# Performance work log

Hardware: AMD Instinct MI355X
Metric: run time of the kernel (lower is better)

## Reference

```python
import jax, jax.numpy as jnp
import numpy as np
from jax import lax

B, T, D, H, L, F, K, G = 4, 1024, 1024, 16, 4, 4096, 128, 16
HD = D // H
EPS = 1e-5

def _ln(x, s, b):
    m = jnp.mean(x, axis=-1, keepdims=True)
    v = jnp.mean(jnp.square(x - m), axis=-1, keepdims=True)
    return (x - m) * lax.rsqrt(v + EPS) * s + b

def setup_inputs() -> dict:
    key = jax.random.key(0)
    ks = jax.random.split(key, 16)
    s = 0.02
    rn = lambda k, sh: jax.random.normal(k, sh, dtype=jnp.float32)
    return {
        "x": rn(ks[0], (B, T, D)),
        "position_bias": rn(ks[1], (H, T, T)) * 0.1,
        "conv_w": rn(ks[2], (D, D // G, K)) * s,  # torch Conv1d OIH layout
        "conv_b": jnp.zeros((D,), jnp.float32),
        "ln0_s": jnp.ones((D,), jnp.float32),
        "ln0_b": jnp.zeros((D,), jnp.float32),
        "qkv_w": rn(ks[3], (L, D, 3 * D)) * s,
        "qkv_b": jnp.zeros((L, 3 * D), jnp.float32),
        "out_w": rn(ks[4], (L, D, D)) * s,
        "out_b": jnp.zeros((L, D), jnp.float32),
        "gru_w": rn(ks[5], (L, HD, 8)) * s,
        "gru_b": jnp.zeros((L, 8), jnp.float32),
        "gru_c": jnp.ones((L, 1, H, 1, 1), jnp.float32),
        "ln1_s": jnp.ones((L, D), jnp.float32),
        "ln1_b": jnp.zeros((L, D), jnp.float32),
        "ffn_w1": rn(ks[6], (L, D, F)) * s,
        "ffn_b1": jnp.zeros((L, F), jnp.float32),
        "ffn_w2": rn(ks[7], (L, F, D)) * s,
        "ffn_b2": jnp.zeros((L, D), jnp.float32),
        "ln2_s": jnp.ones((L, D), jnp.float32),
        "ln2_b": jnp.zeros((L, D), jnp.float32),
    }

def _conv_pos(x, conv_w, conv_b):
    # x: (B, T, D) -> ConvPositionalEmbedding (non-causal): pad K//2, drop last (K even), GELU
    xc = x.transpose(0, 2, 1)  # (B, D, T)
    y = lax.conv_general_dilated(
        xc, conv_w, window_strides=(1,), padding=[(K // 2, K // 2)],
        dimension_numbers=("NCH", "OIH", "NCH"), feature_group_count=G)
    y = y[..., :-1] + conv_b[None, :, None]  # remove=1 since kernel even
    return jax.nn.gelu(y, approximate=False).transpose(0, 2, 1)

def _layer(x, position_bias, qkv_w, qkv_b, out_w, out_b, gru_w, gru_b, gru_c,
           ln1_s, ln1_b, ffn_w1, ffn_b1, ffn_w2, ffn_b2, ln2_s, ln2_b):
    b, t, _ = x.shape
    qkv = x @ qkv_w + qkv_b                       # (B, T, 3D)
    qkv = qkv.reshape(b, t, 3, H, HD)
    q, k, v = (qkv[:, :, i].transpose(0, 2, 1, 3) for i in range(3))  # (B,H,T,HD)
    # GRU-gated relative position bias
    gi = x.reshape(b, t, H, HD).transpose(0, 2, 1, 3)      # (B,H,T,HD)
    proj = (gi @ gru_w + gru_b).reshape(b, H, t, 2, 4).sum(-1)  # (B,H,T,2)
    g = jax.nn.sigmoid(proj)
    gate_a, gate_b = g[..., :1], g[..., 1:]
    gate = gate_a * (gate_b * gru_c - 1.0) + 2.0            # (B,H,T,1)
    gated_bias = gate * position_bias                       # (B,H,T,T)
    scores = jnp.einsum("bhqd,bhkd->bhqk", q, k) / np.sqrt(HD) + gated_bias
    attn = jax.nn.softmax(scores, axis=-1)
    o = jnp.einsum("bhqk,bhkd->bhqd", attn, v)
    o = o.transpose(0, 2, 1, 3).reshape(b, t, D) @ out_w + out_b
    x = _ln(x + o, ln1_s, ln1_b)
    f = jax.nn.gelu(x @ ffn_w1 + ffn_b1, approximate=False) @ ffn_w2 + ffn_b2
    return _ln(x + f, ln2_s, ln2_b)

def reference(x, position_bias, conv_w, conv_b, ln0_s, ln0_b, qkv_w, qkv_b,
              out_w, out_b, gru_w, gru_b, gru_c, ln1_s, ln1_b,
              ffn_w1, ffn_b1, ffn_w2, ffn_b2, ln2_s, ln2_b):
    x = x + _conv_pos(x, conv_w, conv_b)
    x = _ln(x, ln0_s, ln0_b)
    for i in range(L):
        x = _layer(x, position_bias, qkv_w[i], qkv_b[i], out_w[i], out_b[i],
                   gru_w[i], gru_b[i], gru_c[i], ln1_s[i], ln1_b[i],
                   ffn_w1[i], ffn_b1[i], ffn_w2[i], ffn_b2[i], ln2_s[i], ln2_b[i])
    return x
```

## Files before the change

kernel.cpp:

```cpp
#include <hip/hip_runtime.h>
#include <hip/hip_bf16.h>
#include <math.h>

#define B_ 4
#define T_ 1024
#define D_ 1024
#define H_ 16
#define HD_ 64
#define L_ 4
#define F_ 4096
#define KC_ 128
#define G_ 16

typedef __attribute__((ext_vector_type(8))) short bf16x8;
typedef __attribute__((ext_vector_type(4))) float f32x4;

__device__ __forceinline__ float bf2f(unsigned short h){ return __uint_as_float(((unsigned int)h)<<16); }
__device__ __forceinline__ unsigned short f2bf(float f){
  unsigned int u = __float_as_uint(f);
  unsigned int r = u + 0x7fffu + ((u>>16)&1u);
  return (unsigned short)(r>>16);
}
__device__ __forceinline__ float gelu_exact(float v){ return 0.5f*v*(1.0f+erff(v*0.70710678118654752f)); }
__device__ __forceinline__ bool is_f32d(const unsigned short* disc){ return disc[0] == 0; }
__device__ __forceinline__ float dynload(const void* p, long long i, bool f32){
  return f32 ? ((const float*)p)[i] : bf2f(((const unsigned short*)p)[i]);
}
__device__ __forceinline__ void gl2lds16(const void* g, void* l){
  __builtin_amdgcn_global_load_lds((const __attribute__((address_space(1))) void*)g,
                                   (__attribute__((address_space(3))) void*)l, 16, 0, 0);
}

__global__ __launch_bounds__(256)
void cvt_bf16(const void* __restrict__ src, unsigned short* __restrict__ dst,
              const unsigned short* __restrict__ disc)
{
  const bool f32 = is_f32d(disc);
  long long i0 = ((long long)blockIdx.x*256 + threadIdx.x)*8;
  if (f32){
    #pragma unroll
    for (int j=0;j<8;j++) dst[i0+j] = f2bf(((const float*)src)[i0+j]);
  } else {
    *(uint4*)&dst[i0] = *(const uint4*)(&((const unsigned short*)src)[i0]);
  }
}

template<int ACT>
__global__ __launch_bounds__(256)
void gemm_bt(const unsigned short* __restrict__ A, long long lda,
             const unsigned short* __restrict__ Bt, long long ldb,
             unsigned short* __restrict__ C, long long ldc,
             const void* __restrict__ bias,
             const unsigned short* __restrict__ disc, long long biasOff,
             int M, int N, int Kd,
             long long aZ, long long bZ, long long cZ)
{
  A  += (long long)blockIdx.z * aZ;
  Bt += (long long)blockIdx.z * bZ;
  C  += (long long)blockIdx.z * cZ;
  const int n0 = blockIdx.x * 128;
  const int m0 = blockIdx.y * 128;
  __shared__ unsigned short As[128*32];
  __shared__ unsigned short Bs[128*32];
  const int tid  = threadIdx.x;
  const int lane = tid & 63;
  const int wave = tid >> 6;
  const int wm = (wave >> 1) * 64;
  const int wn = (wave & 1) * 64;
  const int lm = lane & 15;
  const int lq = lane >> 4;
  f32x4 acc[4][4];
  #pragma unroll
  for (int i=0;i<4;i++)
    #pragma unroll
    for (int j=0;j<4;j++) acc[i][j] = (f32x4){0.f,0.f,0.f,0.f};

  const int sr = tid >> 2;
  const int sk = (tid & 3) * 8;
  for (int k0 = 0; k0 < Kd; k0 += 32) {
    __syncthreads();
    int b0r = n0 + sr;      if (b0r > N-1) b0r = N-1;
    int b1r = n0 + 64 + sr; if (b1r > N-1) b1r = N-1;
    gl2lds16(&A [(long long)(m0 + sr)      * lda + k0 + sk], &As[tid*8]);
    gl2lds16(&A [(long long)(m0 + 64 + sr) * lda + k0 + sk], &As[2048 + tid*8]);
    gl2lds16(&Bt[(long long)b0r * ldb + k0 + sk],            &Bs[tid*8]);
    gl2lds16(&Bt[(long long)b1r * ldb + k0 + sk],            &Bs[2048 + tid*8]);
    __syncthreads();
    bf16x8 af[4], bfr[4];
    #pragma unroll
    for (int i=0;i<4;i++){
      af[i]  = *(const bf16x8*)&As[(wm + i*16 + lm)*32 + lq*8];
      bfr[i] = *(const bf16x8*)&Bs[(wn + i*16 + lm)*32 + lq*8];
    }
    #pragma unroll
    for (int mi=0;mi<4;mi++)
      #pragma unroll
      for (int ni=0;ni<4;ni++)
        acc[mi][ni] = __builtin_amdgcn_mfma_f32_16x16x32_bf16(af[mi], bfr[ni], acc[mi][ni], 0, 0, 0);
  }
  const bool f32 = is_f32d(disc);
  #pragma unroll
  for (int ni=0;ni<4;ni++){
    int gn = n0 + wn + ni*16 + lm;
    if (gn >= N) continue;
    float bv = bias ? dynload(bias, biasOff + gn, f32) : 0.f;
    #pragma unroll
    for (int mi=0;mi<4;mi++){
      int gm = m0 + wm + mi*16 + lq*4;
      #pragma unroll
      for (int r=0;r<4;r++){
        float v = acc[mi][ni][r] + bv;
        if (ACT==1) v = gelu_exact(v);
        C[(long long)(gm + r) * ldc + gn] = f2bf(v);
      }
    }
  }
}

__global__ __launch_bounds__(256)
void transpose2d(const void* __restrict__ in, long long irs, long long inZ,
                 unsigned short* __restrict__ out, long long ors, long long outZ,
                 const unsigned short* __restrict__ disc, long long eoff)
{
  const bool f32 = disc ? is_f32d(disc) : false;
  const unsigned short* in16 = (const unsigned short*)in;
  const float* in32 = (const float*)in;
  const long long zoff = eoff + (long long)blockIdx.z * inZ;
  out += (long long)blockIdx.z * outZ;
  __shared__ unsigned short tile[64][65];
  const int c0 = blockIdx.x * 64;
  const int r0 = blockIdx.y * 64;
  const int tid = threadIdx.x;
  const int tr = tid >> 4;
  const int tc = (tid & 15) * 4;
  #pragma unroll
  for (int i=0;i<4;i++){
    long long base = zoff + (long long)(r0 + tr + i*16) * irs + c0 + tc;
    #pragma unroll
    for (int j=0;j<4;j++)
      tile[tr + i*16][tc+j] = f32 ? f2bf(in32[base+j]) : in16[base+j];
  }
  __syncthreads();
  #pragma unroll
  for (int i=0;i<4;i++){
    unsigned short* q = out + (long long)(c0 + tr + i*16) * ors + r0 + tc;
    q[0] = tile[tc+0][tr + i*16];
    q[1] = tile[tc+1][tr + i*16];
    q[2] = tile[tc+2][tr + i*16];
    q[3] = tile[tc+3][tr + i*16];
  }
}

__global__ __launch_bounds__(256)
void convw_transform(const void* __restrict__ cw, unsigned short* __restrict__ cwT,
                     const unsigned short* __restrict__ disc)
{
  const bool f32 = is_f32d(disc);
  const int o = blockIdx.x;
  __shared__ unsigned short lds[8192];
  const long long base = (long long)o*8192;
  for (int idx=threadIdx.x; idx<8192; idx+=256)
    lds[idx] = f32 ? f2bf(((const float*)cw)[base+idx]) : ((const unsigned short*)cw)[base+idx];
  __syncthreads();
  for (int idx=threadIdx.x; idx<8192; idx+=256){
    int k = idx >> 6, ic = idx & 63;
    cwT[((long long)k<<16) + (o<<6) + ic] = lds[ic*128 + k];
  }
}

__global__ __launch_bounds__(256)
void conv_mfma(const unsigned short* __restrict__ x,
               const unsigned short* __restrict__ cwT,
               const void* __restrict__ cb,
               unsigned short* __restrict__ out,
               const unsigned short* __restrict__ disc)
{
  const int g  = blockIdx.x;
  const int t0 = blockIdx.y * 128;
  const int b  = blockIdx.z;
  __shared__ unsigned short xs[255*72];
  __shared__ unsigned short wbuf[2*64*72];
  const int tid  = threadIdx.x;
  const int lane = tid & 63;
  const int wave = tid >> 6;
  const int lm = lane & 15;
  const int lq = lane >> 4;

  for (int c = tid; c < 255*8; c += 256){
    int row = c >> 3, icc = (c & 7) * 8;
    int t = t0 - 64 + row;
    uint4 v = {0,0,0,0};
    if (t >= 0 && t < T_) v = *(const uint4*)&x[((long long)b*T_ + t)*D_ + (g<<6) + icc];
    *(uint4*)&xs[row*72 + icc] = v;
  }

  f32x4 acc[2][4];
  #pragma unroll
  for (int i=0;i<2;i++)
    #pragma unroll
    for (int j=0;j<4;j++) acc[i][j] = (f32x4){0.f,0.f,0.f,0.f};

  uint4 wreg[4];
  #pragma unroll
  for (int j=0;j<4;j++){
    int cc = j*256 + tid;
    int tapL = cc >> 9, rem = cc & 511;
    wreg[j] = *(const uint4*)&cwT[((long long)tapL<<16) + (g<<12) + rem*8];
  }

  for (int it = 0; it < 64; it++){
    __syncthreads();
    #pragma unroll
    for (int j=0;j<4;j++){
      int cc = j*256 + tid;
      int tapL = cc >> 9, rem = cc & 511;
      int o = rem >> 3, icc = (rem & 7) * 8;
      *(uint4*)&wbuf[(tapL*64 + o)*72 + icc] = wreg[j];
    }
    __syncthreads();
    if (it < 63){
      int tapBase = (it+1)*2;
      #pragma unroll
      for (int j=0;j<4;j++){
        int cc = j*256 + tid;
        int tapL = cc >> 9, rem = cc & 511;
        wreg[j] = *(const uint4*)&cwT[((long long)(tapBase+tapL)<<16) + (g<<12) + rem*8];
      }
    }
    #pragma unroll
    for (int tl=0; tl<2; tl++){
      int tap = it*2 + tl;
      #pragma unroll
      for (int ks=0; ks<2; ks++){
        bf16x8 a0 = *(const bf16x8*)&xs[(wave*32      + lm + tap)*72 + ks*32 + lq*8];
        bf16x8 a1 = *(const bf16x8*)&xs[(wave*32 + 16 + lm + tap)*72 + ks*32 + lq*8];
        #pragma unroll
        for (int ni=0; ni<4; ni++){
          bf16x8 bf = *(const bf16x8*)&wbuf[(tl*64 + ni*16 + lm)*72 + ks*32 + lq*8];
          acc[0][ni] = __builtin_amdgcn_mfma_f32_16x16x32_bf16(a0, bf, acc[0][ni], 0, 0, 0);
          acc[1][ni] = __builtin_amdgcn_mfma_f32_16x16x32_bf16(a1, bf, acc[1][ni], 0, 0, 0);
        }
      }
    }
  }

  const bool f32 = is_f32d(disc);
  float bv[4];
  #pragma unroll
  for (int ni=0; ni<4; ni++) bv[ni] = dynload(cb, (g<<6) + ni*16 + lm, f32);
  #pragma unroll
  for (int mt=0; mt<2; mt++){
    #pragma unroll
    for (int r=0; r<4; r++){
      int t = t0 + wave*32 + mt*16 + lq*4 + r;
      long long base = ((long long)b*T_ + t)*D_ + (g<<6);
      #pragma unroll
      for (int ni=0; ni<4; ni++){
        int o = ni*16 + lm;
        float val = acc[mt][ni][r] + bv[ni];
        float xv  = bf2f(x[base + o]);
        out[base + o] = f2bf(xv + gelu_exact(val));
      }
    }
  }
}

__global__ __launch_bounds__(256)
void add_ln(const unsigned short* __restrict__ a,
            const unsigned short* __restrict__ bAdd,
            const void* __restrict__ s, const void* __restrict__ bi,
            void* __restrict__ out,
            const unsigned short* __restrict__ disc, int dynOut, long long eoff)
{
  const bool f32 = is_f32d(disc);
  const long long row = blockIdx.x;
  const int tid = threadIdx.x;
  __shared__ float red[8];
  float v[4];
  uint2 ua = *(const uint2*)&a[row*D_ + tid*4];
  unsigned short t4[4]; *(uint2*)t4 = ua;
  v[0]=bf2f(t4[0]); v[1]=bf2f(t4[1]); v[2]=bf2f(t4[2]); v[3]=bf2f(t4[3]);
  if (bAdd){
    uint2 ub = *(const uint2*)&bAdd[row*D_ + tid*4];
    *(uint2*)t4 = ub;
    v[0]+=bf2f(t4[0]); v[1]+=bf2f(t4[1]); v[2]+=bf2f(t4[2]); v[3]+=bf2f(t4[3]);
  }
  float sum = v[0]+v[1]+v[2]+v[3];
  float sq  = v[0]*v[0]+v[1]*v[1]+v[2]*v[2]+v[3]*v[3];
  #pragma unroll
  for (int off=32; off>=1; off>>=1){
    sum += __shfl_xor(sum, off);
    sq  += __shfl_xor(sq,  off);
  }
  const int wv = tid>>6;
  if ((tid&63)==0){ red[wv] = sum; red[4+wv] = sq; }
  __syncthreads();
  sum = red[0]+red[1]+red[2]+red[3];
  sq  = red[4]+red[5]+red[6]+red[7];
  float mean = sum * (1.0f/D_);
  float var  = sq * (1.0f/D_) - mean*mean;
  float rstd = rsqrtf(var + 1e-5f);
  #pragma unroll
  for (int i=0;i<4;i++){
    float sv = dynload(s, eoff + tid*4+i, f32);
    float bv = dynload(bi, eoff + tid*4+i, f32);
    float ov = (v[i]-mean)*rstd*sv + bv;
    if (dynOut && f32) ((float*)out)[row*D_ + tid*4 + i] = ov;
    else ((unsigned short*)out)[row*D_ + tid*4 + i] = f2bf(ov);
  }
}

__global__ __launch_bounds__(256)
void gate_kernel(const unsigned short* __restrict__ x,
                 const void* __restrict__ gw, const void* __restrict__ gb,
                 const void* __restrict__ gc, float* __restrict__ gate,
                 const unsigned short* __restrict__ disc,
                 long long wOff, long long bOff, long long cOff)
{
  const bool f32 = is_f32d(disc);
  int r = blockIdx.x*4 + (threadIdx.x>>6);
  int lane = threadIdx.x & 63;
  int b = r >> 14;
  int h = (r >> 10) & 15;
  int t = r & 1023;
  float xv = bf2f(x[((long long)b*T_ + t)*D_ + h*64 + lane]);
  float w0=0.f, w1=0.f;
  #pragma unroll
  for (int j=0;j<4;j++) w0 += dynload(gw, wOff + lane*8+j, f32);
  #pragma unroll
  for (int j=4;j<8;j++) w1 += dynload(gw, wOff + lane*8+j, f32);
  float p0 = xv*w0, p1 = xv*w1;
  #pragma unroll
  for (int off=32; off>=1; off>>=1){
    p0 += __shfl_xor(p0, off);
    p1 += __shfl_xor(p1, off);
  }
  if (lane==0){
    float b0=0.f, b1=0.f;
    #pragma unroll
    for (int j=0;j<4;j++) b0 += dynload(gb, bOff + j, f32);
    #pragma unroll
    for (int j=4;j<8;j++) b1 += dynload(gb, bOff + j, f32);
    float s0 = p0 + b0, s1 = p1 + b1;
    float ga  = 1.f/(1.f+expf(-s0));
    float gbv = 1.f/(1.f+expf(-s1));
    float c = dynload(gc, cOff + h, f32);
    gate[r] = ga*(gbv*c - 1.0f) + 2.0f;
  }
}

__global__ __launch_bounds__(256)
void attn_fused(const unsigned short* __restrict__ qkv,
                const unsigned short* __restrict__ vT,
                const void* __restrict__ pb,
                const float* __restrict__ gate,
                unsigned short* __restrict__ o,
                const unsigned short* __restrict__ disc)
{
  const int q0 = blockIdx.x * 64;
  const int h  = blockIdx.y;
  const int b  = blockIdx.z;
  const bool f32 = is_f32d(disc);
  __shared__ unsigned short Ks[64*72];
  __shared__ unsigned short Vs[64*72];
  __shared__ unsigned short Ps[64*72];
  const int tid  = threadIdx.x;
  const int lane = tid & 63;
  const int wave = tid >> 6;
  const int lm = lane & 15;
  const int lq = lane >> 4;

  bf16x8 qa[2];
  {
    const unsigned short* qrow = &qkv[((long long)b*T_ + q0 + wave*16 + lm)*3*D_ + h*64];
    qa[0] = *(const bf16x8*)&qrow[lq*8];
    qa[1] = *(const bf16x8*)&qrow[32 + lq*8];
  }
  float g4[4];
  #pragma unroll
  for (int r=0;r<4;r++)
    g4[r] = gate[((long long)(b*H_ + h))*T_ + q0 + wave*16 + lq*4 + r];

  float m[4] = {-3.0e38f,-3.0e38f,-3.0e38f,-3.0e38f};
  float l[4] = {0.f,0.f,0.f,0.f};
  f32x4 oacc[4];
  #pragma unroll
  for (int ni=0;ni<4;ni++) oacc[ni] = (f32x4){0.f,0.f,0.f,0.f};

  const unsigned short* kbase = &qkv[((long long)b*T_)*3*D_ + D_ + h*64];
  const unsigned short* vtb   = &vT[((long long)b*H_ + h)*64*T_];
  const long long pbrow = ((long long)h*T_ + q0 + wave*16 + lq*4)*T_;

  for (int kv0 = 0; kv0 < T_; kv0 += 64){
    __syncthreads();
    #pragma unroll
    for (int jj=0; jj<2; jj++){
      int cc = jj*256 + tid;
      int row = cc >> 3, icc = (cc & 7)*8;
      *(uint4*)&Ks[row*72 + icc] = *(const uint4*)&kbase[(long long)(kv0+row)*3*D_ + icc];
    }
    #pragma unroll
    for (int jj=0; jj<2; jj++){
      int cc = jj*256 + tid;
      int row = cc >> 3, icc = (cc & 7)*8;
      *(uint4*)&Vs[row*72 + icc] = *(const uint4*)&vtb[(long long)row*T_ + kv0 + icc];
    }
    __syncthreads();
    f32x4 s[4];
    #pragma unroll
    for (int ni=0;ni<4;ni++){
      s[ni] = (f32x4){0.f,0.f,0.f,0.f};
      bf16x8 kb0 = *(const bf16x8*)&Ks[(ni*16+lm)*72 + lq*8];
      bf16x8 kb1 = *(const bf16x8*)&Ks[(ni*16+lm)*72 + 32 + lq*8];
      s[ni] = __builtin_amdgcn_mfma_f32_16x16x32_bf16(qa[0], kb0, s[ni], 0, 0, 0);
      s[ni] = __builtin_amdgcn_mfma_f32_16x16x32_bf16(qa[1], kb1, s[ni], 0, 0, 0);
    }
    #pragma unroll
    for (int ni=0;ni<4;ni++)
      #pragma unroll
      for (int r=0;r<4;r++)
        s[ni][r] = s[ni][r]*0.125f + g4[r]*dynload(pb, pbrow + (long long)r*T_ + kv0 + ni*16 + lm, f32);
    #pragma unroll
    for (int r=0;r<4;r++){
      float mx = fmaxf(fmaxf(s[0][r],s[1][r]), fmaxf(s[2][r],s[3][r]));
      mx = fmaxf(mx, __shfl_xor(mx,1));
      mx = fmaxf(mx, __shfl_xor(mx,2));
      mx = fmaxf(mx, __shfl_xor(mx,4));
      mx = fmaxf(mx, __shfl_xor(mx,8));
      float mn = fmaxf(m[r], mx);
      float sc = __expf(m[r]-mn);
      m[r] = mn;
      float rs = 0.f;
      #pragma unroll
      for (int ni=0;ni<4;ni++){
        float e = __expf(s[ni][r]-mn);
        s[ni][r] = e;
        rs += e;
      }
      rs += __shfl_xor(rs,1); rs += __shfl_xor(rs,2);
      rs += __shfl_xor(rs,4); rs += __shfl_xor(rs,8);
      l[r] = l[r]*sc + rs;
      #pragma unroll
      for (int ni=0;ni<4;ni++) oacc[ni][r] *= sc;
    }
    #pragma unroll
    for (int ni=0;ni<4;ni++)
      #pragma unroll
      for (int r=0;r<4;r++)
        Ps[(wave*16+lq*4+r)*72 + ni*16+lm] = f2bf(s[ni][r]);
    bf16x8 pa0 = *(const bf16x8*)&Ps[(wave*16+lm)*72 + lq*8];
    bf16x8 pa1 = *(const bf16x8*)&Ps[(wave*16+lm)*72 + 32 + lq*8];
    #pragma unroll
    for (int ni=0;ni<4;ni++){
      bf16x8 vb0 = *(const bf16x8*)&Vs[(ni*16+lm)*72 + lq*8];
      bf16x8 vb1 = *(const bf16x8*)&Vs[(ni*16+lm)*72 + 32 + lq*8];
      oacc[ni] = __builtin_amdgcn_mfma_f32_16x16x32_bf16(pa0, vb0, oacc[ni], 0, 0, 0);
      oacc[ni] = __builtin_amdgcn_mfma_f32_16x16x32_bf16(pa1, vb1, oacc[ni], 0, 0, 0);
    }
  }
  #pragma unroll
  for (int r=0;r<4;r++){
    float inv = 1.0f / l[r];
    int q = q0 + wave*16 + lq*4 + r;
    #pragma unroll
    for (int ni=0;ni<4;ni++)
      o[((long long)b*T_ + q)*D_ + h*64 + ni*16 + lm] = f2bf(oacc[ni][r]*inv);
  }
}

extern "C" void kernel_launch(void* const* d_in, const int* in_sizes, int n_in,
                              void* d_out, int out_size, void* d_ws, size_t ws_size,
                              hipStream_t stream)
{
  (void)in_sizes; (void)n_in; (void)out_size; (void)ws_size;
  const void* x_in     = d_in[0];
  const void* pos_bias = d_in[1];
  const void* conv_w   = d_in[2];
  const void* conv_b   = d_in[3];
  const unsigned short* disc = (const unsigned short*)d_in[4];
  const void* ln0_s    = d_in[4];
  const void* ln0_b    = d_in[5];
  const void* qkv_w    = d_in[6];
  const void* qkv_b    = d_in[7];
  const void* out_w    = d_in[8];
  const void* out_b    = d_in[9];
  const void* gru_w    = d_in[10];
  const void* gru_b    = d_in[11];
  const void* gru_c    = d_in[12];
  const void* ln1_s    = d_in[13];
  const void* ln1_b    = d_in[14];
  const void* ffn_w1   = d_in[15];
  const void* ffn_b1   = d_in[16];
  const void* ffn_w2   = d_in[17];
  const void* ffn_b2   = d_in[18];
  const void* ln2_s    = d_in[19];
  const void* ln2_b    = d_in[20];

  const size_t MB = (size_t)1<<20;
  char* ws = (char*)d_ws;
  unsigned short* xcvt   = (unsigned short*)(ws);
  unsigned short* xbuf   = (unsigned short*)(ws +   8*MB);
  unsigned short* qkvbuf = (unsigned short*)(ws +  16*MB);
  unsigned short* obuf   = (unsigned short*)(ws +  40*MB);
  unsigned short* hs     = (unsigned short*)(ws +  48*MB);
  unsigned short* wT     = (unsigned short*)(ws +  80*MB);
  float*          gateb  = (float*)         (ws + 106*MB);

  dim3 blk(256);

  cvt_bf16<<<dim3((B_*T_*D_)/2048), blk, 0, stream>>>(x_in, xcvt, disc);
  convw_transform<<<dim3(1024), blk, 0, stream>>>(conv_w, wT, disc);
  conv_mfma<<<dim3(G_, T_/128, B_), blk, 0, stream>>>(xcvt, wT, conv_b, xbuf, disc);
  add_ln<<<dim3(B_*T_), blk, 0, stream>>>(xbuf, nullptr, ln0_s, ln0_b, xbuf, disc, 0, 0);

  for (int l=0; l<L_; l++){
    unsigned short* qkvT = wT;
    unsigned short* outT = wT + (size_t)3*1024*1024;
    unsigned short* w1T  = wT + (size_t)4*1024*1024;
    unsigned short* w2T  = wT + (size_t)8*1024*1024;
    unsigned short* vTall = hs;
    transpose2d<<<dim3(48,16,1), blk, 0, stream>>>(qkv_w, 3*D_, 0, qkvT, D_, 0, disc, (long long)l*D_*3*D_);
    transpose2d<<<dim3(16,16,1), blk, 0, stream>>>(out_w, D_,   0, outT, D_, 0, disc, (long long)l*D_*D_);
    transpose2d<<<dim3(64,16,1), blk, 0, stream>>>(ffn_w1, F_,  0, w1T,  D_, 0, disc, (long long)l*D_*F_);
    transpose2d<<<dim3(16,64,1), blk, 0, stream>>>(ffn_w2, D_,  0, w2T,  F_, 0, disc, (long long)l*F_*D_);

    gate_kernel<<<dim3(B_*H_*T_/4), blk, 0, stream>>>(xbuf, gru_w, gru_b, gru_c, gateb, disc,
                                                      (long long)l*HD_*8, (long long)l*8, (long long)l*H_);

    gemm_bt<0><<<dim3(24,32,1), blk, 0, stream>>>(xbuf, D_, qkvT, D_, qkvbuf, 3*D_, qkv_b, disc, (long long)l*3*D_,
                                                  B_*T_, 3*D_, D_, 0,0,0);
    for (int b=0;b<B_;b++)
      transpose2d<<<dim3(1,16,16), blk, 0, stream>>>(qkvbuf + (long long)b*T_*3*D_ + 2*D_, 3*D_, 64,
                                                     vTall + (long long)b*H_*64*T_, T_, (long long)64*T_,
                                                     nullptr, 0);
    attn_fused<<<dim3(T_/64, H_, B_), blk, 0, stream>>>(qkvbuf, vTall, pos_bias, gateb, obuf, disc);

    gemm_bt<0><<<dim3(8,32,1), blk, 0, stream>>>(obuf, D_, outT, D_, qkvbuf, D_, out_b, disc, (long long)l*D_,
                                                 B_*T_, D_, D_, 0,0,0);
    add_ln<<<dim3(B_*T_), blk, 0, stream>>>(xbuf, qkvbuf, ln1_s, ln1_b, xbuf, disc, 0, (long long)l*D_);
    gemm_bt<1><<<dim3(32,32,1), blk, 0, stream>>>(xbuf, D_, w1T, D_, hs, F_, ffn_b1, disc, (long long)l*F_,
                                                  B_*T_, F_, D_, 0,0,0);
    gemm_bt<0><<<dim3(8,32,1), blk, 0, stream>>>(hs, F_, w2T, F_, qkvbuf, D_, ffn_b2, disc, (long long)l*D_,
                                                 B_*T_, D_, F_, 0,0,0);
    void* dst = (l==L_-1) ? d_out : (void*)xbuf;
    add_ln<<<dim3(B_*T_), blk, 0, stream>>>(xbuf, qkvbuf, ln2_s, ln2_b, dst, disc, (l==L_-1)?1:0, (long long)l*D_);
  }
}
```

Measured before the change: 2.254 ms.

## Fuse gate, conversion and transposes into fewer launches; add 128x64 GEMM tile

New measurement: 1.875 ms. 16.8% less time.

```diff
diff --git a/kernel.cpp b/kernel.cpp
--- a/kernel.cpp
+++ b/kernel.cpp
@@ -29,20 +29,6 @@
 __device__ __forceinline__ void gl2lds16(const void* g, void* l){
   __builtin_amdgcn_global_load_lds((const __attribute__((address_space(1))) void*)g,
                                    (__attribute__((address_space(3))) void*)l, 16, 0, 0);
-}
-
-__global__ __launch_bounds__(256)
-void cvt_bf16(const void* __restrict__ src, unsigned short* __restrict__ dst,
-              const unsigned short* __restrict__ disc)
-{
-  const bool f32 = is_f32d(disc);
-  long long i0 = ((long long)blockIdx.x*256 + threadIdx.x)*8;
-  if (f32){
-    #pragma unroll
-    for (int j=0;j<8;j++) dst[i0+j] = f2bf(((const float*)src)[i0+j]);
-  } else {
-    *(uint4*)&dst[i0] = *(const uint4*)(&((const unsigned short*)src)[i0]);
-  }
 }
 
 template<int ACT>
@@ -117,25 +103,96 @@
   }
 }
 
-__global__ __launch_bounds__(256)
-void transpose2d(const void* __restrict__ in, long long irs, long long inZ,
-                 unsigned short* __restrict__ out, long long ors, long long outZ,
-                 const unsigned short* __restrict__ disc, long long eoff)
-{
-  const bool f32 = disc ? is_f32d(disc) : false;
+template<int ACT>
+__global__ __launch_bounds__(256)
+void gemm_bt64(const unsigned short* __restrict__ A, long long lda,
+               const unsigned short* __restrict__ Bt, long long ldb,
+               unsigned short* __restrict__ C, long long ldc,
+               const void* __restrict__ bias,
+               const unsigned short* __restrict__ disc, long long biasOff,
+               int M, int N, int Kd)
+{
+  const int n0 = blockIdx.x * 64;
+  const int m0 = blockIdx.y * 128;
+  __shared__ unsigned short As[128*32];
+  __shared__ unsigned short Bs[64*32];
+  const int tid  = threadIdx.x;
+  const int lane = tid & 63;
+  const int wave = tid >> 6;
+  const int wm = wave * 32;
+  const int lm = lane & 15;
+  const int lq = lane >> 4;
+  f32x4 acc[2][4];
+  #pragma unroll
+  for (int i=0;i<2;i++)
+    #pragma unroll
+    for (int j=0;j<4;j++) acc[i][j] = (f32x4){0.f,0.f,0.f,0.f};
+
+  const int sr = tid >> 2;
+  const int sk = (tid & 3) * 8;
+  for (int k0 = 0; k0 < Kd; k0 += 32) {
+    __syncthreads();
+    gl2lds16(&A [(long long)(m0 + sr)      * lda + k0 + sk], &As[tid*8]);
+    gl2lds16(&A [(long long)(m0 + 64 + sr) * lda + k0 + sk], &As[2048 + tid*8]);
+    gl2lds16(&Bt[(long long)(n0 + sr)      * ldb + k0 + sk], &Bs[tid*8]);
+    __syncthreads();
+    bf16x8 af[2], bfr[4];
+    #pragma unroll
+    for (int i=0;i<2;i++) af[i]  = *(const bf16x8*)&As[(wm + i*16 + lm)*32 + lq*8];
+    #pragma unroll
+    for (int i=0;i<4;i++) bfr[i] = *(const bf16x8*)&Bs[(i*16 + lm)*32 + lq*8];
+    #pragma unroll
+    for (int mi=0;mi<2;mi++)
+      #pragma unroll
+      for (int ni=0;ni<4;ni++)
+        acc[mi][ni] = __builtin_amdgcn_mfma_f32_16x16x32_bf16(af[mi], bfr[ni], acc[mi][ni], 0, 0, 0);
+  }
+  const bool f32 = is_f32d(disc);
+  #pragma unroll
+  for (int ni=0;ni<4;ni++){
+    int gn = n0 + ni*16 + lm;
+    if (gn >= N) continue;
+    float bv = bias ? dynload(bias, biasOff + gn, f32) : 0.f;
+    #pragma unroll
+    for (int mi=0;mi<2;mi++){
+      int gm = m0 + wm + mi*16 + lq*4;
+      #pragma unroll
+      for (int r=0;r<4;r++){
+        float v = acc[mi][ni][r] + bv;
+        if (ACT==1) v = gelu_exact(v);
+        C[(long long)(gm + r) * ldc + gn] = f2bf(v);
+      }
+    }
+  }
+}
+
+__global__ __launch_bounds__(256)
+void transpose_weights(const void* __restrict__ qkv_w, const void* __restrict__ out_w,
+                       const void* __restrict__ w1, const void* __restrict__ w2,
+                       unsigned short* __restrict__ qkvT, unsigned short* __restrict__ outT,
+                       unsigned short* __restrict__ w1T, unsigned short* __restrict__ w2T,
+                       const unsigned short* __restrict__ disc, int l)
+{
+  const bool f32 = is_f32d(disc);
+  const int id = blockIdx.x;
+  const void* in; unsigned short* out; long long irs, ors, eoff; int c0, r0;
+  if (id < 768){        in=qkv_w; out=qkvT; irs=3072; ors=1024; eoff=(long long)l*D_*3*D_;
+                        c0=(id%48)*64; r0=(id/48)*64; }
+  else if (id < 1024){  int t=id-768;  in=out_w; out=outT; irs=1024; ors=1024; eoff=(long long)l*D_*D_;
+                        c0=(t&15)*64; r0=(t>>4)*64; }
+  else if (id < 2048){  int t=id-1024; in=w1; out=w1T; irs=4096; ors=1024; eoff=(long long)l*D_*F_;
+                        c0=(t&63)*64; r0=(t>>6)*64; }
+  else {                int t=id-2048; in=w2; out=w2T; irs=1024; ors=4096; eoff=(long long)l*F_*D_;
+                        c0=(t&15)*64; r0=(t>>4)*64; }
   const unsigned short* in16 = (const unsigned short*)in;
   const float* in32 = (const float*)in;
-  const long long zoff = eoff + (long long)blockIdx.z * inZ;
-  out += (long long)blockIdx.z * outZ;
   __shared__ unsigned short tile[64][65];
-  const int c0 = blockIdx.x * 64;
-  const int r0 = blockIdx.y * 64;
   const int tid = threadIdx.x;
   const int tr = tid >> 4;
   const int tc = (tid & 15) * 4;
   #pragma unroll
   for (int i=0;i<4;i++){
-    long long base = zoff + (long long)(r0 + tr + i*16) * irs + c0 + tc;
+    long long base = eoff + (long long)(r0 + tr + i*16) * irs + c0 + tc;
     #pragma unroll
     for (int j=0;j<4;j++)
       tile[tr + i*16][tc+j] = f32 ? f2bf(in32[base+j]) : in16[base+j];
@@ -152,34 +209,64 @@
 }
 
 __global__ __launch_bounds__(256)
-void convw_transform(const void* __restrict__ cw, unsigned short* __restrict__ cwT,
+void vt_all(const unsigned short* __restrict__ qkv, unsigned short* __restrict__ vT)
+{
+  const int t0 = blockIdx.x * 64;
+  const int h  = blockIdx.y;
+  const int b  = blockIdx.z;
+  __shared__ unsigned short tile[64][65];
+  const int tid = threadIdx.x;
+  const int tr = tid >> 4;
+  const int tc = (tid & 15) * 4;
+  #pragma unroll
+  for (int i=0;i<4;i++){
+    long long base = ((long long)b*T_ + t0 + tr + i*16)*3*D_ + 2*D_ + h*64 + tc;
+    #pragma unroll
+    for (int j=0;j<4;j++) tile[tr + i*16][tc+j] = qkv[base+j];
+  }
+  __syncthreads();
+  #pragma unroll
+  for (int i=0;i<4;i++){
+    unsigned short* q = vT + ((long long)(b*H_ + h)*64 + tr + i*16)*T_ + t0 + tc;
+    q[0] = tile[tc+0][tr + i*16];
+    q[1] = tile[tc+1][tr + i*16];
+    q[2] = tile[tc+2][tr + i*16];
+    q[3] = tile[tc+3][tr + i*16];
+  }
+}
+
+__global__ __launch_bounds__(256)
+void convw_transform(const void* __restrict__ cw, unsigned short* __restrict__ cwF,
                      const unsigned short* __restrict__ disc)
 {
   const bool f32 = is_f32d(disc);
   const int o = blockIdx.x;
+  const int g = o >> 6, ni = (o >> 4) & 3, lm = o & 15;
   __shared__ unsigned short lds[8192];
   const long long base = (long long)o*8192;
   for (int idx=threadIdx.x; idx<8192; idx+=256)
     lds[idx] = f32 ? f2bf(((const float*)cw)[base+idx]) : ((const unsigned short*)cw)[base+idx];
   __syncthreads();
   for (int idx=threadIdx.x; idx<8192; idx+=256){
-    int k = idx >> 6, ic = idx & 63;
-    cwT[((long long)k<<16) + (o<<6) + ic] = lds[ic*128 + k];
-  }
-}
-
-__global__ __launch_bounds__(256)
-void conv_mfma(const unsigned short* __restrict__ x,
-               const unsigned short* __restrict__ cwT,
+    int tap = idx >> 6, ic = idx & 63;
+    int ks = ic >> 5, lq = (ic >> 3) & 3, j = ic & 7;
+    cwF[((long long)(tap*16 + g) << 12) + (ks << 11) + (ni << 9) + ((lq*16 + lm) * 8) + j]
+      = lds[ic*128 + tap];
+  }
+}
+
+__global__ __launch_bounds__(256)
+void conv_mfma(const void* __restrict__ x,
+               const unsigned short* __restrict__ cwF,
                const void* __restrict__ cb,
                unsigned short* __restrict__ out,
                const unsigned short* __restrict__ disc)
 {
+  const bool f32 = is_f32d(disc);
   const int g  = blockIdx.x;
   const int t0 = blockIdx.y * 128;
   const int b  = blockIdx.z;
   __shared__ unsigned short xs[255*72];
-  __shared__ unsigned short wbuf[2*64*72];
   const int tid  = threadIdx.x;
   const int lane = tid & 63;
   const int wave = tid >> 6;
@@ -189,9 +276,20 @@
   for (int c = tid; c < 255*8; c += 256){
     int row = c >> 3, icc = (c & 7) * 8;
     int t = t0 - 64 + row;
-    uint4 v = {0,0,0,0};
-    if (t >= 0 && t < T_) v = *(const uint4*)&x[((long long)b*T_ + t)*D_ + (g<<6) + icc];
-    *(uint4*)&xs[row*72 + icc] = v;
+    unsigned short v8[8];
+    if (t >= 0 && t < T_){
+      long long bb = ((long long)b*T_ + t)*D_ + (g<<6) + icc;
+      if (f32){
+        #pragma unroll
+        for (int j=0;j<8;j++) v8[j] = f2bf(((const float*)x)[bb+j]);
+      } else {
+        *(uint4*)v8 = *(const uint4*)&((const unsigned short*)x)[bb];
+      }
+    } else {
+      #pragma unroll
+      for (int j=0;j<8;j++) v8[j] = 0;
+    }
+    *(uint4*)&xs[row*72 + icc] = *(uint4*)v8;
   }
 
   f32x4 acc[2][4];
@@ -200,51 +298,25 @@
     #pragma unroll
     for (int j=0;j<4;j++) acc[i][j] = (f32x4){0.f,0.f,0.f,0.f};
 
-  uint4 wreg[4];
-  #pragma unroll
-  for (int j=0;j<4;j++){
-    int cc = j*256 + tid;
-    int tapL = cc >> 9, rem = cc & 511;
-    wreg[j] = *(const uint4*)&cwT[((long long)tapL<<16) + (g<<12) + rem*8];
-  }
-
-  for (int it = 0; it < 64; it++){
-    __syncthreads();
-    #pragma unroll
-    for (int j=0;j<4;j++){
-      int cc = j*256 + tid;
-      int tapL = cc >> 9, rem = cc & 511;
-      int o = rem >> 3, icc = (rem & 7) * 8;
-      *(uint4*)&wbuf[(tapL*64 + o)*72 + icc] = wreg[j];
-    }
-    __syncthreads();
-    if (it < 63){
-      int tapBase = (it+1)*2;
-      #pragma unroll
-      for (int j=0;j<4;j++){
-        int cc = j*256 + tid;
-        int tapL = cc >> 9, rem = cc & 511;
-        wreg[j] = *(const uint4*)&cwT[((long long)(tapBase+tapL)<<16) + (g<<12) + rem*8];
+  __syncthreads();
+
+  const unsigned short* wg = cwF + ((long long)g << 12);
+  #pragma unroll 2
+  for (int tap = 0; tap < 128; tap++){
+    const unsigned short* wt = wg + ((long long)tap << 16);
+    #pragma unroll
+    for (int ks=0; ks<2; ks++){
+      bf16x8 a0 = *(const bf16x8*)&xs[(wave*32      + lm + tap)*72 + ks*32 + lq*8];
+      bf16x8 a1 = *(const bf16x8*)&xs[(wave*32 + 16 + lm + tap)*72 + ks*32 + lq*8];
+      #pragma unroll
+      for (int ni=0; ni<4; ni++){
+        bf16x8 bf = *(const bf16x8*)&wt[(ks<<11) + (ni<<9) + lane*8];
+        acc[0][ni] = __builtin_amdgcn_mfma_f32_16x16x32_bf16(a0, bf, acc[0][ni], 0, 0, 0);
+        acc[1][ni] = __builtin_amdgcn_mfma_f32_16x16x32_bf16(a1, bf, acc[1][ni], 0, 0, 0);
       }
     }
-    #pragma unroll
-    for (int tl=0; tl<2; tl++){
-      int tap = it*2 + tl;
-      #pragma unroll
-      for (int ks=0; ks<2; ks++){
-        bf16x8 a0 = *(const bf16x8*)&xs[(wave*32      + lm + tap)*72 + ks*32 + lq*8];
-        bf16x8 a1 = *(const bf16x8*)&xs[(wave*32 + 16 + lm + tap)*72 + ks*32 + lq*8];
-        #pragma unroll
-        for (int ni=0; ni<4; ni++){
-          bf16x8 bf = *(const bf16x8*)&wbuf[(tl*64 + ni*16 + lm)*72 + ks*32 + lq*8];
-          acc[0][ni] = __builtin_amdgcn_mfma_f32_16x16x32_bf16(a0, bf, acc[0][ni], 0, 0, 0);
-          acc[1][ni] = __builtin_amdgcn_mfma_f32_16x16x32_bf16(a1, bf, acc[1][ni], 0, 0, 0);
-        }
-      }
-    }
-  }
-
-  const bool f32 = is_f32d(disc);
+  }
+
   float bv[4];
   #pragma unroll
   for (int ni=0; ni<4; ni++) bv[ni] = dynload(cb, (g<<6) + ni*16 + lm, f32);
@@ -253,13 +325,13 @@
     #pragma unroll
     for (int r=0; r<4; r++){
       int t = t0 + wave*32 + mt*16 + lq*4 + r;
-      long long base = ((long long)b*T_ + t)*D_ + (g<<6);
+      long long bb = ((long long)b*T_ + t)*D_ + (g<<6);
       #pragma unroll
       for (int ni=0; ni<4; ni++){
         int o = ni*16 + lm;
         float val = acc[mt][ni][r] + bv[ni];
-        float xv  = bf2f(x[base + o]);
-        out[base + o] = f2bf(xv + gelu_exact(val));
+        float xv  = f32 ? ((const float*)x)[bb + o] : bf2f(((const unsigned short*)x)[bb + o]);
+        out[bb + o] = f2bf(xv + gelu_exact(val));
       }
     }
   }
@@ -311,51 +383,14 @@
 }
 
 __global__ __launch_bounds__(256)
-void gate_kernel(const unsigned short* __restrict__ x,
-                 const void* __restrict__ gw, const void* __restrict__ gb,
-                 const void* __restrict__ gc, float* __restrict__ gate,
-                 const unsigned short* __restrict__ disc,
-                 long long wOff, long long bOff, long long cOff)
-{
-  const bool f32 = is_f32d(disc);
-  int r = blockIdx.x*4 + (threadIdx.x>>6);
-  int lane = threadIdx.x & 63;
-  int b = r >> 14;
-  int h = (r >> 10) & 15;
-  int t = r & 1023;
-  float xv = bf2f(x[((long long)b*T_ + t)*D_ + h*64 + lane]);
-  float w0=0.f, w1=0.f;
-  #pragma unroll
-  for (int j=0;j<4;j++) w0 += dynload(gw, wOff + lane*8+j, f32);
-  #pragma unroll
-  for (int j=4;j<8;j++) w1 += dynload(gw, wOff + lane*8+j, f32);
-  float p0 = xv*w0, p1 = xv*w1;
-  #pragma unroll
-  for (int off=32; off>=1; off>>=1){
-    p0 += __shfl_xor(p0, off);
-    p1 += __shfl_xor(p1, off);
-  }
-  if (lane==0){
-    float b0=0.f, b1=0.f;
-    #pragma unroll
-    for (int j=0;j<4;j++) b0 += dynload(gb, bOff + j, f32);
-    #pragma unroll
-    for (int j=4;j<8;j++) b1 += dynload(gb, bOff + j, f32);
-    float s0 = p0 + b0, s1 = p1 + b1;
-    float ga  = 1.f/(1.f+expf(-s0));
-    float gbv = 1.f/(1.f+expf(-s1));
-    float c = dynload(gc, cOff + h, f32);
-    gate[r] = ga*(gbv*c - 1.0f) + 2.0f;
-  }
-}
-
-__global__ __launch_bounds__(256)
 void attn_fused(const unsigned short* __restrict__ qkv,
                 const unsigned short* __restrict__ vT,
                 const void* __restrict__ pb,
-                const float* __restrict__ gate,
+                const unsigned short* __restrict__ x,
+                const void* __restrict__ gw, const void* __restrict__ gb, const void* __restrict__ gc,
                 unsigned short* __restrict__ o,
-                const unsigned short* __restrict__ disc)
+                const unsigned short* __restrict__ disc,
+                long long wOff, long long bOff, long long cOff)
 {
   const int q0 = blockIdx.x * 64;
   const int h  = blockIdx.y;
@@ -364,12 +399,54 @@
   __shared__ unsigned short Ks[64*72];
   __shared__ unsigned short Vs[64*72];
   __shared__ unsigned short Ps[64*72];
+  __shared__ float w0s[64], w1s[64], gsh[64];
   const int tid  = threadIdx.x;
   const int lane = tid & 63;
   const int wave = tid >> 6;
   const int lm = lane & 15;
   const int lq = lane >> 4;
 
+  if (tid < 64){
+    float s0 = 0.f, s1 = 0.f;
+    #pragma unroll
+    for (int j=0;j<4;j++) s0 += dynload(gw, wOff + tid*8 + j, f32);
+    #pragma unroll
+    for (int j=4;j<8;j++) s1 += dynload(gw, wOff + tid*8 + j, f32);
+    w0s[tid] = s0; w1s[tid] = s1;
+  }
+  __syncthreads();
+  {
+    int row = tid >> 2, dq = (tid & 3) * 16;
+    const unsigned short* xr = &x[((long long)b*T_ + q0 + row)*D_ + h*64 + dq];
+    bf16x8 xa = *(const bf16x8*)&xr[0];
+    bf16x8 xb = *(const bf16x8*)&xr[8];
+    float p0 = 0.f, p1 = 0.f;
+    #pragma unroll
+    for (int k=0;k<8;k++){
+      float xv = bf2f((unsigned short)xa[k]);
+      p0 += xv * w0s[dq+k]; p1 += xv * w1s[dq+k];
+    }
+    #pragma unroll
+    for (int k=0;k<8;k++){
+      float xv = bf2f((unsigned short)xb[k]);
+      p0 += xv * w0s[dq+8+k]; p1 += xv * w1s[dq+8+k];
+    }
+    p0 += __shfl_xor(p0,1); p0 += __shfl_xor(p0,2);
+    p1 += __shfl_xor(p1,1); p1 += __shfl_xor(p1,2);
+    if ((tid & 3) == 0){
+      float b0=0.f, b1=0.f;
+      #pragma unroll
+      for (int j=0;j<4;j++) b0 += dynload(gb, bOff + j, f32);
+      #pragma unroll
+      for (int j=4;j<8;j++) b1 += dynload(gb, bOff + j, f32);
+      float ga  = 1.f/(1.f+expf(-(p0+b0)));
+      float gbv = 1.f/(1.f+expf(-(p1+b1)));
+      float c = dynload(gc, cOff + h, f32);
+      gsh[row] = ga*(gbv*c - 1.0f) + 2.0f;
+    }
+  }
+  __syncthreads();
+
   bf16x8 qa[2];
   {
     const unsigned short* qrow = &qkv[((long long)b*T_ + q0 + wave*16 + lm)*3*D_ + h*64];
@@ -378,8 +455,7 @@
   }
   float g4[4];
   #pragma unroll
-  for (int r=0;r<4;r++)
-    g4[r] = gate[((long long)(b*H_ + h))*T_ + q0 + wave*16 + lq*4 + r];
+  for (int r=0;r<4;r++) g4[r] = gsh[wave*16 + lq*4 + r];
 
   float m[4] = {-3.0e38f,-3.0e38f,-3.0e38f,-3.0e38f};
   float l[4] = {0.f,0.f,0.f,0.f};
@@ -498,19 +574,16 @@
 
   const size_t MB = (size_t)1<<20;
   char* ws = (char*)d_ws;
-  unsigned short* xcvt   = (unsigned short*)(ws);
   unsigned short* xbuf   = (unsigned short*)(ws +   8*MB);
   unsigned short* qkvbuf = (unsigned short*)(ws +  16*MB);
   unsigned short* obuf   = (unsigned short*)(ws +  40*MB);
   unsigned short* hs     = (unsigned short*)(ws +  48*MB);
   unsigned short* wT     = (unsigned short*)(ws +  80*MB);
-  float*          gateb  = (float*)         (ws + 106*MB);
 
   dim3 blk(256);
 
-  cvt_bf16<<<dim3((B_*T_*D_)/2048), blk, 0, stream>>>(x_in, xcvt, disc);
   convw_transform<<<dim3(1024), blk, 0, stream>>>(conv_w, wT, disc);
-  conv_mfma<<<dim3(G_, T_/128, B_), blk, 0, stream>>>(xcvt, wT, conv_b, xbuf, disc);
+  conv_mfma<<<dim3(G_, T_/128, B_), blk, 0, stream>>>(x_in, wT, conv_b, xbuf, disc);
   add_ln<<<dim3(B_*T_), blk, 0, stream>>>(xbuf, nullptr, ln0_s, ln0_b, xbuf, disc, 0, 0);
 
   for (int l=0; l<L_; l++){
@@ -519,29 +592,24 @@
     unsigned short* w1T  = wT + (size_t)4*1024*1024;
     unsigned short* w2T  = wT + (size_t)8*1024*1024;
     unsigned short* vTall = hs;
-    transpose2d<<<dim3(48,16,1), blk, 0, stream>>>(qkv_w, 3*D_, 0, qkvT, D_, 0, disc, (long long)l*D_*3*D_);
-    transpose2d<<<dim3(16,16,1), blk, 0, stream>>>(out_w, D_,   0, outT, D_, 0, disc, (long long)l*D_*D_);
-    transpose2d<<<dim3(64,16,1), blk, 0, stream>>>(ffn_w1, F_,  0, w1T,  D_, 0, disc, (long long)l*D_*F_);
-    transpose2d<<<dim3(16,64,1), blk, 0, stream>>>(ffn_w2, D_,  0, w2T,  F_, 0, disc, (long long)l*F_*D_);
-
-    gate_kernel<<<dim3(B_*H_*T_/4), blk, 0, stream>>>(xbuf, gru_w, gru_b, gru_c, gateb, disc,
-                                                      (long long)l*HD_*8, (long long)l*8, (long long)l*H_);
+
+    transpose_weights<<<dim3(3072), blk, 0, stream>>>(qkv_w, out_w, ffn_w1, ffn_w2,
+                                                      qkvT, outT, w1T, w2T, disc, l);
 
     gemm_bt<0><<<dim3(24,32,1), blk, 0, stream>>>(xbuf, D_, qkvT, D_, qkvbuf, 3*D_, qkv_b, disc, (long long)l*3*D_,
                                                   B_*T_, 3*D_, D_, 0,0,0);
-    for (int b=0;b<B_;b++)
-      transpose2d<<<dim3(1,16,16), blk, 0, stream>>>(qkvbuf + (long long)b*T_*3*D_ + 2*D_, 3*D_, 64,
-                                                     vTall + (long long)b*H_*64*T_, T_, (long long)64*T_,
-                                                     nullptr, 0);
-    attn_fused<<<dim3(T_/64, H_, B_), blk, 0, stream>>>(qkvbuf, vTall, pos_bias, gateb, obuf, disc);
-
-    gemm_bt<0><<<dim3(8,32,1), blk, 0, stream>>>(obuf, D_, outT, D_, qkvbuf, D_, out_b, disc, (long long)l*D_,
-                                                 B_*T_, D_, D_, 0,0,0);
+    vt_all<<<dim3(T_/64, H_, B_), blk, 0, stream>>>(qkvbuf, vTall);
+    attn_fused<<<dim3(T_/64, H_, B_), blk, 0, stream>>>(qkvbuf, vTall, pos_bias, xbuf,
+                                                        gru_w, gru_b, gru_c, obuf, disc,
+                                                        (long long)l*HD_*8, (long long)l*8, (long long)l*H_);
+
+    gemm_bt64<0><<<dim3(16,32,1), blk, 0, stream>>>(obuf, D_, outT, D_, qkvbuf, D_, out_b, disc, (long long)l*D_,
+                                                    B_*T_, D_, D_);
     add_ln<<<dim3(B_*T_), blk, 0, stream>>>(xbuf, qkvbuf, ln1_s, ln1_b, xbuf, disc, 0, (long long)l*D_);
     gemm_bt<1><<<dim3(32,32,1), blk, 0, stream>>>(xbuf, D_, w1T, D_, hs, F_, ffn_b1, disc, (long long)l*F_,
                                                   B_*T_, F_, D_, 0,0,0);
-    gemm_bt<0><<<dim3(8,32,1), blk, 0, stream>>>(hs, F_, w2T, F_, qkvbuf, D_, ffn_b2, disc, (long long)l*D_,
-                                                 B_*T_, D_, F_, 0,0,0);
+    gemm_bt64<0><<<dim3(16,32,1), blk, 0, stream>>>(hs, F_, w2T, F_, qkvbuf, D_, ffn_b2, disc, (long long)l*D_,
+                                                    B_*T_, D_, F_);
     void* dst = (l==L_-1) ? d_out : (void*)xbuf;
     add_ln<<<dim3(B_*T_), blk, 0, stream>>>(xbuf, qkvbuf, ln2_s, ln2_b, dst, disc, (l==L_-1)?1:0, (long long)l*D_);
   }
```
